# Kernel optimization log

Measured on AMD Instinct MI355X. Metric: run time of the kernel, lower is better.

The kernel has to match this reference:

```python
import jax, jax.numpy as jnp
import numpy as np

N, P1, P2, D = 4, 8192, 8192, 3
BIG = 1e10  # masks out padded target points before top-k (pytorch3d uses +inf)


def setup_inputs() -> dict:
    key = jax.random.key(0)
    k1, k2, k3 = jax.random.split(key, 3)
    pred_points = jax.random.normal(k1, (N, P1, D), dtype=jnp.float32)
    target_points = jax.random.normal(k2, (N, P2, D), dtype=jnp.float32)
    # ragged target lengths in [P2//2, P2] (always > 0 so every batch element is 'visible')
    target_lengths = jax.random.randint(k3, (N,), P2 // 2, P2 + 1, dtype=jnp.int32)
    return {
        "pred_points": pred_points,
        "target_points": target_points,
        "target_lengths": target_lengths,
        "num_neighbours": 1,
    }


def reference(pred_points, target_points, target_lengths, num_neighbours):
    x, y = pred_points, target_points  # [N,P1,D], [N,P2,D]
    n, p1, _ = x.shape
    p2 = y.shape[1]
    x2 = jnp.sum(x * x, axis=-1)
    y2 = jnp.sum(y * y, axis=-1)
    d2 = x2[:, :, None] + y2[:, None, :] - 2.0 * jnp.einsum('nid,njd->nij', x, y)
    d2 = jnp.maximum(d2, 0.0)

    # mask of invalid (padded) target points per batch: j >= target_lengths[b]
    y_pad = jnp.arange(p2)[None, :] >= target_lengths[:, None]  # [N,P2]

    # knn_points(x -> y): invalid y columns pushed to BIG before top-k smallest
    dxy = jnp.where(y_pad[:, None, :], BIG, d2)
    nn_x = -jax.lax.top_k(-dxy, num_neighbours)[0]          # [N,P1,K]
    cham_x = jnp.sum(jnp.mean(nn_x, axis=-1), axis=1) / p1  # point_reduction='mean'

    # knn_points(y -> x): all x points valid; zero out padded y rows afterwards
    dyx = jnp.swapaxes(d2, 1, 2)                            # [N,P2,P1]
    nn_y = -jax.lax.top_k(-dyx, num_neighbours)[0]          # [N,P2,K]
    cham_y_pts = jnp.where(y_pad, 0.0, jnp.mean(nn_y, axis=-1))
    cham_y = jnp.sum(cham_y_pts, axis=1) / target_lengths.astype(x.dtype)

    # batch_reduction='mean'
    loss = (jnp.sum(cham_x) + jnp.sum(cham_y)) / n
    return loss
```

## Files before the change

### kernel.cpp

```cpp
#include <hip/hip_runtime.h>


typedef _Float16 f16;
typedef _Float16 half8 __attribute__((ext_vector_type(8)));
typedef float f32x4 __attribute__((ext_vector_type(4)));

constexpr int N = 4;
constexpr int P = 8192;
constexpr int NSEG = 8;
constexpr int SEGC = P / NSEG;
constexpr int BROWS = 256;
constexpr int RBLK = P / BROWS;
constexpr float BIGV = 1e30f;

__global__ __launch_bounds__(256) void chamfer_prep(
    const float* __restrict__ pred, const float* __restrict__ targ,
    f16* __restrict__ rowP, f16* __restrict__ colP,
    f16* __restrict__ rowT, f16* __restrict__ colT)
{
    const int idx = blockIdx.x * 256 + threadIdx.x;
    const f16 one = (f16)1.0f;
    const half8 vz = {0, 0, 0, 0, 0, 0, 0, 0};
    #pragma unroll
    for (int which = 0; which < 2; ++which) {
        const float* s = (which ? targ : pred) + (size_t)idx * 3;
        half8* rdst = (half8*)((which ? rowT : rowP) + (size_t)idx * 32);
        half8* cdst = (half8*)((which ? colT : colP) + (size_t)idx * 32);
        const float x0 = s[0], x1 = s[1], x2 = s[2];
        const float w = fmaf(x0, x0, fmaf(x1, x1, x2 * x2));
        const f16 h0 = (f16)x0, h1 = (f16)x1, h2 = (f16)x2;
        const f16 l0 = (f16)(x0 - (float)h0), l1 = (f16)(x1 - (float)h1), l2 = (f16)(x2 - (float)h2);
        const f16 wh = (f16)w, wl = (f16)(w - (float)wh);
        half8 r0 = {h0, h1, h2, l0, l1, l2, h0, h1};
        half8 r1 = {h2, wh, wl, one, one, l0, l1, l2};
        rdst[0] = r0; rdst[1] = r1; rdst[2] = vz; rdst[3] = vz;
        const f16 n0 = (f16)(-2.0f * (float)h0), n1 = (f16)(-2.0f * (float)h1), n2 = (f16)(-2.0f * (float)h2);
        const f16 u0 = (f16)(-2.0f * (float)l0), u1 = (f16)(-2.0f * (float)l1), u2 = (f16)(-2.0f * (float)l2);
        half8 c0v = {n0, n1, n2, n0, n1, n2, u0, u1};
        half8 c1v = {u2, one, one, wh, wl, u0, u1, u2};
        cdst[0] = c0v; cdst[1] = c1v; cdst[2] = vz; cdst[3] = vz;
    }
}

__global__ __launch_bounds__(256) void chamfer_pass(
    const f16* __restrict__ rowP, const f16* __restrict__ colP,
    const f16* __restrict__ rowT, const f16* __restrict__ colT,
    const int* __restrict__ lens, float* __restrict__ part)
{
    const int H   = blockIdx.x;
    const int Lid = (H & 7) * 256 + (H >> 3);
    const int rb   = Lid & (RBLK - 1);
    const int b    = (Lid >> 5) & (N - 1);
    const int seg  = (Lid >> 8) & (NSEG - 1);
    const int pass = Lid >> 11;
    const int segf = (Lid >> 7) & (NSEG - 1);
    const int passf = Lid >> 10;

    const int L    = lens[b];
    const int Lcol = passf ? P : L;
    const int tid  = threadIdx.x;
    const int w    = tid >> 6;
    const int lane = tid & 63;
    const int q    = lane >> 4;
    const int cc   = lane & 15;
    const int row0 = rb * BROWS + w * 64;
    const int c0   = segf * SEGC;

    float* brow = part + (((size_t)passf * N + b) * NSEG + segf) * P + rb * BROWS;

    if (c0 >= Lcol) {
        brow[tid] = BIGV;
        return;
    }
    if (passf && row0 >= L) return;

    const f16* ab = (passf ? rowT : rowP) + (size_t)b * (P * 32);
    const f16* bb = (passf ? colP : colT) + (size_t)b * (P * 32);

    half8 afr[4];
    #pragma unroll
    for (int it = 0; it < 4; ++it)
        afr[it] = *(const half8*)(ab + (size_t)(row0 + it * 16 + cc) * 32 + q * 8);

    float rowacc[4][4];
    #pragma unroll
    for (int it = 0; it < 4; ++it)
        #pragma unroll
        for (int r = 0; r < 4; ++r) rowacc[it][r] = BIGV;

    const int Ll   = Lcol - c0;
    const int Lloc = (Ll < SEGC) ? Ll : SEGC;
    int njs        = (Lloc + 63) >> 6;

    const f32x4 zz = {0.f, 0.f, 0.f, 0.f};
    const f16* bptr = bb + (size_t)cc * 32 + q * 8;
    int cbase = c0;

    half8 b0[4], b1[4];
    #pragma unroll
    for (int f = 0; f < 4; ++f)
        b0[f] = *(const half8*)(bptr + (size_t)cbase * 32 + f * 512);

    auto STEP = [&](half8 (&cur)[4], half8 (&nxt)[4]) {
        const int cn = (cbase + 64 < P) ? (cbase + 64) : cbase;
        #pragma unroll
        for (int f = 0; f < 4; ++f)
            nxt[f] = *(const half8*)(bptr + (size_t)cn * 32 + f * 512);
        if (cbase + 64 <= Lcol) {
            #pragma unroll
            for (int f = 0; f < 4; ++f)
                #pragma unroll
                for (int it = 0; it < 4; ++it) {
                    const f32x4 d = __builtin_amdgcn_mfma_f32_16x16x32_f16(afr[it], cur[f], zz, 0, 0, 0);
                    #pragma unroll
                    for (int r = 0; r < 4; ++r)
                        rowacc[it][r] = fminf(rowacc[it][r], d[r]);
                }
        } else {
            #pragma unroll
            for (int f = 0; f < 4; ++f) {
                const bool val = (cbase + f * 16 + cc) < Lcol;
                #pragma unroll
                for (int it = 0; it < 4; ++it) {
                    const f32x4 d = __builtin_amdgcn_mfma_f32_16x16x32_f16(afr[it], cur[f], zz, 0, 0, 0);
                    #pragma unroll
                    for (int r = 0; r < 4; ++r)
                        rowacc[it][r] = fminf(rowacc[it][r], val ? d[r] : BIGV);
                }
            }
        }
        cbase += 64;
    };

    while (njs >= 2) { STEP(b0, b1); STEP(b1, b0); njs -= 2; }
    if (njs) STEP(b0, b1);

    float* wrow = brow + w * 64;
    #pragma unroll
    for (int it = 0; it < 4; ++it) {
        #pragma unroll
        for (int r = 0; r < 4; ++r) {
            float v = rowacc[it][r];
            v = fminf(v, __shfl_xor(v, 1, 64));
            v = fminf(v, __shfl_xor(v, 2, 64));
            v = fminf(v, __shfl_xor(v, 4, 64));
            v = fminf(v, __shfl_xor(v, 8, 64));
            rowacc[it][r] = v;
        }
        if (cc == 0) {
            f32x4 o = {rowacc[it][0], rowacc[it][1], rowacc[it][2], rowacc[it][3]};
            *(f32x4*)(wrow + it * 16 + q * 4) = o;
        }
    }
}

__global__ __launch_bounds__(256) void chamfer_reduce(
    const float* __restrict__ part, const int* __restrict__ lens,
    float* __restrict__ out)
{
    const int item = blockIdx.x * 256 + threadIdx.x;
    const int dir = item >> 15;
    const int b   = (item >> 13) & (N - 1);
    const int p   = item & (P - 1);
    const int L   = lens[b];

    float c = 0.f;
    if (dir == 0) {
        const float* base = part + ((size_t)b * NSEG) * P + p;
        float v = base[0];
        #pragma unroll
        for (int s = 1; s < NSEG; ++s) v = fminf(v, base[(size_t)s * P]);
        c = fmaxf(v, 0.f) * (1.0f / ((float)P * (float)N));
    } else if (p < L) {
        const float* base = part + (((size_t)N + b) * NSEG) * P + p;
        float v = base[0];
        #pragma unroll
        for (int s = 1; s < NSEG; ++s) v = fminf(v, base[(size_t)s * P]);
        c = fmaxf(v, 0.f) / ((float)L * (float)N);
    }
    #pragma unroll
    for (int off = 32; off; off >>= 1) c += __shfl_down(c, off, 64);
    __shared__ float acc[4];
    if ((threadIdx.x & 63) == 0) acc[threadIdx.x >> 6] = c;
    __syncthreads();
    if (threadIdx.x == 0) atomicAdd(out, acc[0] + acc[1] + acc[2] + acc[3]);
}

extern "C" void kernel_launch(void* const* d_in, const int* in_sizes, int n_in,
                              void* d_out, int out_size, void* d_ws, size_t ws_size,
                              hipStream_t stream)
{
    const float* pred = (const float*)d_in[0];
    const float* targ = (const float*)d_in[1];
    const int*   lens = (const int*)d_in[2];
    float* out = (float*)d_out;
    char*  ws  = (char*)d_ws;

    const size_t packb = (size_t)N * P * 32 * sizeof(f16);
    f16*   rowP = (f16*)ws;
    f16*   colP = (f16*)(ws + packb);
    f16*   rowT = (f16*)(ws + 2 * packb);
    f16*   colT = (f16*)(ws + 3 * packb);
    float* part = (float*)(ws + 4 * packb);

    hipMemsetAsync(out, 0, out_size * sizeof(float), stream);
    chamfer_prep<<<(N * P) / 256, 256, 0, stream>>>(pred, targ, rowP, colP, rowT, colT);
    chamfer_pass<<<2 * N * RBLK * NSEG, 256, 0, stream>>>(rowP, colP, rowT, colT, lens, part);
    chamfer_reduce<<<(2 * N * P) / 256, 256, 0, stream>>>(part, lens, out);
}
```

Before: 111.9 us.

## Switch to 32x32x16 MFMA with compact packing and ragged-aware work scheduling

Packed row/column operands shrink from 32 to 16 halves per point, and the distance tiles now use the 32x32x16 f16 MFMA instead of 16x16x32, which halves the K padding waste. Work units are assigned per wave by a dynamic mapping over the ragged target lengths, so only the needed row/column tiles are launched and columns beyond each batch's length are skipped. Invalid tail columns are masked through a sentinel fragment holding the f16 maximum, and loads use triple buffering. The reduce kernel reads only the active chunks for pass 0. This adds index-mapping complexity and risks exceeding the fixed 2048-block grid or misplacing outputs.

Result: slower. 166.6 us (+49.0%).

```diff
diff --git a/kernel.cpp b/kernel.cpp
--- a/kernel.cpp
+++ b/kernel.cpp
@@ -3,14 +3,10 @@
 
 typedef _Float16 f16;
 typedef _Float16 half8 __attribute__((ext_vector_type(8)));
-typedef float f32x4 __attribute__((ext_vector_type(4)));
+typedef float f32x16 __attribute__((ext_vector_type(16)));
 
 constexpr int N = 4;
 constexpr int P = 8192;
-constexpr int NSEG = 8;
-constexpr int SEGC = P / NSEG;
-constexpr int BROWS = 256;
-constexpr int RBLK = P / BROWS;
 constexpr float BIGV = 1e30f;
 
 __global__ __launch_bounds__(256) void chamfer_prep(
@@ -20,12 +16,11 @@
 {
     const int idx = blockIdx.x * 256 + threadIdx.x;
     const f16 one = (f16)1.0f;
-    const half8 vz = {0, 0, 0, 0, 0, 0, 0, 0};
     #pragma unroll
     for (int which = 0; which < 2; ++which) {
         const float* s = (which ? targ : pred) + (size_t)idx * 3;
-        half8* rdst = (half8*)((which ? rowT : rowP) + (size_t)idx * 32);
-        half8* cdst = (half8*)((which ? colT : colP) + (size_t)idx * 32);
+        half8* rdst = (half8*)((which ? rowT : rowP) + (size_t)idx * 16);
+        half8* cdst = (half8*)((which ? colT : colP) + (size_t)idx * 16);
         const float x0 = s[0], x1 = s[1], x2 = s[2];
         const float w = fmaf(x0, x0, fmaf(x1, x1, x2 * x2));
         const f16 h0 = (f16)x0, h1 = (f16)x1, h2 = (f16)x2;
@@ -33,12 +28,12 @@
         const f16 wh = (f16)w, wl = (f16)(w - (float)wh);
         half8 r0 = {h0, h1, h2, l0, l1, l2, h0, h1};
         half8 r1 = {h2, wh, wl, one, one, l0, l1, l2};
-        rdst[0] = r0; rdst[1] = r1; rdst[2] = vz; rdst[3] = vz;
+        rdst[0] = r0; rdst[1] = r1;
         const f16 n0 = (f16)(-2.0f * (float)h0), n1 = (f16)(-2.0f * (float)h1), n2 = (f16)(-2.0f * (float)h2);
         const f16 u0 = (f16)(-2.0f * (float)l0), u1 = (f16)(-2.0f * (float)l1), u2 = (f16)(-2.0f * (float)l2);
         half8 c0v = {n0, n1, n2, n0, n1, n2, u0, u1};
         half8 c1v = {u2, one, one, wh, wl, u0, u1, u2};
-        cdst[0] = c0v; cdst[1] = c1v; cdst[2] = vz; cdst[3] = vz;
+        cdst[0] = c0v; cdst[1] = c1v;
     }
 }
 
@@ -49,107 +44,116 @@
 {
     const int H   = blockIdx.x;
     const int Lid = (H & 7) * 256 + (H >> 3);
-    const int rb   = Lid & (RBLK - 1);
-    const int b    = (Lid >> 5) & (N - 1);
-    const int seg  = (Lid >> 8) & (NSEG - 1);
-    const int pass = Lid >> 11;
-    const int segf = (Lid >> 7) & (NSEG - 1);
-    const int passf = Lid >> 10;
-
-    const int L    = lens[b];
-    const int Lcol = passf ? P : L;
     const int tid  = threadIdx.x;
     const int w    = tid >> 6;
     const int lane = tid & 63;
-    const int q    = lane >> 4;
-    const int cc   = lane & 15;
-    const int row0 = rb * BROWS + w * 64;
-    const int c0   = segf * SEGC;
-
-    float* brow = part + (((size_t)passf * N + b) * NSEG + segf) * P + rb * BROWS;
-
-    if (c0 >= Lcol) {
-        brow[tid] = BIGV;
-        return;
-    }
-    if (passf && row0 >= L) return;
-
-    const f16* ab = (passf ? rowT : rowP) + (size_t)b * (P * 32);
-    const f16* bb = (passf ? colP : colT) + (size_t)b * (P * 32);
-
-    half8 afr[4];
-    #pragma unroll
-    for (int it = 0; it < 4; ++it)
-        afr[it] = *(const half8*)(ab + (size_t)(row0 + it * 16 + cc) * 32 + q * 8);
-
-    float rowacc[4][4];
-    #pragma unroll
-    for (int it = 0; it < 4; ++it)
-        #pragma unroll
-        for (int r = 0; r < 4; ++r) rowacc[it][r] = BIGV;
-
-    const int Ll   = Lcol - c0;
-    const int Lloc = (Ll < SEGC) ? Ll : SEGC;
-    int njs        = (Lloc + 63) >> 6;
-
-    const f32x4 zz = {0.f, 0.f, 0.f, 0.f};
-    const f16* bptr = bb + (size_t)cc * 32 + q * 8;
-    int cbase = c0;
-
-    half8 b0[4], b1[4];
-    #pragma unroll
-    for (int f = 0; f < 4; ++f)
-        b0[f] = *(const half8*)(bptr + (size_t)cbase * 32 + f * 512);
-
-    auto STEP = [&](half8 (&cur)[4], half8 (&nxt)[4]) {
-        const int cn = (cbase + 64 < P) ? (cbase + 64) : cbase;
-        #pragma unroll
-        for (int f = 0; f < 4; ++f)
-            nxt[f] = *(const half8*)(bptr + (size_t)cn * 32 + f * 512);
-        if (cbase + 64 <= Lcol) {
-            #pragma unroll
-            for (int f = 0; f < 4; ++f)
-                #pragma unroll
-                for (int it = 0; it < 4; ++it) {
-                    const f32x4 d = __builtin_amdgcn_mfma_f32_16x16x32_f16(afr[it], cur[f], zz, 0, 0, 0);
-                    #pragma unroll
-                    for (int r = 0; r < 4; ++r)
-                        rowacc[it][r] = fminf(rowacc[it][r], d[r]);
-                }
+    const int uid  = Lid * 4 + w;
+    const int lc   = lane & 31;
+    const int kh   = lane >> 5;
+    const int kh8  = kh * 8;
+
+    int Ls[4], CT[4], NC[4];
+    #pragma unroll
+    for (int i = 0; i < 4; ++i) {
+        Ls[i] = lens[i];
+        CT[i] = (Ls[i] + 63) >> 6;
+        NC[i] = (CT[i] + 15) >> 4;
+    }
+    int pass = -1, b = 0, local = uid;
+    #pragma unroll
+    for (int i = 0; i < 8; ++i) {
+        const int sz = (i < 4) ? 128 * NC[i] : CT[i - 4] * 8;
+        if (pass < 0) {
+            if (local < sz) { pass = i >> 2; b = i & 3; }
+            else local -= sz;
+        }
+    }
+    if (pass < 0) return;
+
+    const int L = Ls[b];
+    int ch, tau;
+    if (pass == 0) { ch = local >> 7; tau = local & 127; }
+    else           { ch = local / CT[b]; tau = local - ch * CT[b]; }
+
+    const int row0   = tau * 64;
+    const int cstart = ch * 1024;
+    const int cend0  = CT[b] * 64;
+    const int cend   = pass ? (cstart + 1024)
+                            : ((cstart + 1024 < cend0) ? cstart + 1024 : cend0);
+    const int colLim = pass ? P : L;
+
+    const f16* ab = (pass ? rowT : rowP) + (size_t)b * (P * 16);
+    const f16* bb = (pass ? colP : colT) + (size_t)b * (P * 16);
+    float* wrow = part + (((size_t)pass * N + b) * 8 + ch) * P + row0;
+
+    const half8 afr0 = *(const half8*)(ab + (size_t)(row0 + lc) * 16 + kh8);
+    const half8 afr1 = *(const half8*)(ab + (size_t)(row0 + 32 + lc) * 16 + kh8);
+
+    half8 mfr = {0, 0, 0, 0, 0, 0, 0, 0};
+    if (kh) mfr[3] = (f16)65504.0f;
+
+    float acc0[16], acc1[16];
+    #pragma unroll
+    for (int r = 0; r < 16; ++r) { acc0[r] = BIGV; acc1[r] = BIGV; }
+
+    const f32x16 zz = {0.f,0.f,0.f,0.f, 0.f,0.f,0.f,0.f,
+                       0.f,0.f,0.f,0.f, 0.f,0.f,0.f,0.f};
+
+    auto LOADF = [&](half8* dst, int cb) {
+        if (cb + 64 <= colLim) {
+            dst[0] = *(const half8*)(bb + (size_t)(cb + lc) * 16 + kh8);
+            dst[1] = *(const half8*)(bb + (size_t)(cb + 32 + lc) * 16 + kh8);
         } else {
             #pragma unroll
-            for (int f = 0; f < 4; ++f) {
-                const bool val = (cbase + f * 16 + cc) < Lcol;
-                #pragma unroll
-                for (int it = 0; it < 4; ++it) {
-                    const f32x4 d = __builtin_amdgcn_mfma_f32_16x16x32_f16(afr[it], cur[f], zz, 0, 0, 0);
-                    #pragma unroll
-                    for (int r = 0; r < 4; ++r)
-                        rowacc[it][r] = fminf(rowacc[it][r], val ? d[r] : BIGV);
-                }
+            for (int ct = 0; ct < 2; ++ct) {
+                const int col = cb + ct * 32 + lc;
+                dst[ct] = (col < colLim)
+                    ? *(const half8*)(bb + (size_t)col * 16 + kh8) : mfr;
             }
         }
-        cbase += 64;
     };
-
-    while (njs >= 2) { STEP(b0, b1); STEP(b1, b0); njs -= 2; }
-    if (njs) STEP(b0, b1);
-
-    float* wrow = brow + w * 64;
-    #pragma unroll
-    for (int it = 0; it < 4; ++it) {
-        #pragma unroll
-        for (int r = 0; r < 4; ++r) {
-            float v = rowacc[it][r];
+    auto COMP = [&](const half8* cur) {
+        const f32x16 d0 = __builtin_amdgcn_mfma_f32_32x32x16_f16(afr0, cur[0], zz, 0, 0, 0);
+        const f32x16 d1 = __builtin_amdgcn_mfma_f32_32x32x16_f16(afr0, cur[1], zz, 0, 0, 0);
+        #pragma unroll
+        for (int r = 0; r < 16; ++r)
+            acc0[r] = fminf(fminf(acc0[r], d0[r]), d1[r]);
+        const f32x16 e0 = __builtin_amdgcn_mfma_f32_32x32x16_f16(afr1, cur[0], zz, 0, 0, 0);
+        const f32x16 e1 = __builtin_amdgcn_mfma_f32_32x32x16_f16(afr1, cur[1], zz, 0, 0, 0);
+        #pragma unroll
+        for (int r = 0; r < 16; ++r)
+            acc1[r] = fminf(fminf(acc1[r], e0[r]), e1[r]);
+    };
+
+    half8 B0[2], B1[2], B2[2];
+    int njs = (cend - cstart + 63) >> 6;
+    int c = cstart;
+    LOADF(B0, c);
+    LOADF(B1, c + 64);
+    while (njs >= 3) {
+        LOADF(B2, c + 128);
+        COMP(B0);
+        LOADF(B0, c + 192);
+        COMP(B1);
+        LOADF(B1, c + 256);
+        COMP(B2);
+        c += 192; njs -= 3;
+    }
+    if (njs == 2) { COMP(B0); COMP(B1); }
+    else if (njs == 1) { COMP(B0); }
+
+    #pragma unroll
+    for (int rt = 0; rt < 2; ++rt) {
+        #pragma unroll
+        for (int r = 0; r < 16; ++r) {
+            float v = rt ? acc1[r] : acc0[r];
             v = fminf(v, __shfl_xor(v, 1, 64));
             v = fminf(v, __shfl_xor(v, 2, 64));
             v = fminf(v, __shfl_xor(v, 4, 64));
             v = fminf(v, __shfl_xor(v, 8, 64));
-            rowacc[it][r] = v;
-        }
-        if (cc == 0) {
-            f32x4 o = {rowacc[it][0], rowacc[it][1], rowacc[it][2], rowacc[it][3]};
-            *(f32x4*)(wrow + it * 16 + q * 4) = o;
+            v = fminf(v, __shfl_xor(v, 16, 64));
+            if (lc == 0)
+                wrow[rt * 32 + (r & 3) + 8 * (r >> 2) + 4 * kh] = v;
         }
     }
 }
@@ -166,16 +170,16 @@
 
     float c = 0.f;
     if (dir == 0) {
-        const float* base = part + ((size_t)b * NSEG) * P + p;
+        const int NCb = (((L + 63) >> 6) + 15) >> 4;
+        const float* base = part + ((size_t)b * 8) * P + p;
         float v = base[0];
-        #pragma unroll
-        for (int s = 1; s < NSEG; ++s) v = fminf(v, base[(size_t)s * P]);
+        for (int s = 1; s < NCb; ++s) v = fminf(v, base[(size_t)s * P]);
         c = fmaxf(v, 0.f) * (1.0f / ((float)P * (float)N));
     } else if (p < L) {
-        const float* base = part + (((size_t)N + b) * NSEG) * P + p;
+        const float* base = part + (((size_t)N + b) * 8) * P + p;
         float v = base[0];
         #pragma unroll
-        for (int s = 1; s < NSEG; ++s) v = fminf(v, base[(size_t)s * P]);
+        for (int s = 1; s < 8; ++s) v = fminf(v, base[(size_t)s * P]);
         c = fmaxf(v, 0.f) / ((float)L * (float)N);
     }
     #pragma unroll
@@ -196,7 +200,7 @@
     float* out = (float*)d_out;
     char*  ws  = (char*)d_ws;
 
-    const size_t packb = (size_t)N * P * 32 * sizeof(f16);
+    const size_t packb = (size_t)N * P * 16 * sizeof(f16);
     f16*   rowP = (f16*)ws;
     f16*   colP = (f16*)(ws + packb);
     f16*   rowT = (f16*)(ws + 2 * packb);
@@ -205,6 +209,6 @@
 
     hipMemsetAsync(out, 0, out_size * sizeof(float), stream);
     chamfer_prep<<<(N * P) / 256, 256, 0, stream>>>(pred, targ, rowP, colP, rowT, colT);
-    chamfer_pass<<<2 * N * RBLK * NSEG, 256, 0, stream>>>(rowP, colP, rowT, colT, lens, part);
+    chamfer_pass<<<2048, 256, 0, stream>>>(rowP, colP, rowT, colT, lens, part);
     chamfer_reduce<<<(2 * N * P) / 256, 256, 0, stream>>>(part, lens, out);
 }
```
